# Optimization experiments

Hardware: AMD Instinct MI355X
Metric: run time of the kernel (lower is better)

Reference implementation:

```python
import jax, jax.numpy as jnp
import numpy as np

B = 8192          # batch
D = 256           # feature_dim
H = 64            # num attention heads
HD = D // H       # head_dim = 4
NC, NB, NF, NT = 2048, 2048, 512, 768
NCLS = 26
EPS = 1e-5


def _linear_params(k, out_d, in_d):
    s = 1.0 / np.sqrt(in_d)
    kw, kb = jax.random.split(k)
    W = jax.random.uniform(kw, (out_d, in_d), minval=-s, maxval=s, dtype=jnp.float32)
    b = jax.random.uniform(kb, (out_d,), minval=-s, maxval=s, dtype=jnp.float32)
    return W, b


def setup_inputs() -> dict:
    key = jax.random.key(0)
    ks = jax.random.split(key, 16)
    inp = {
        'x_context': jax.random.normal(ks[0], (B, NC), dtype=jnp.float32),
        'x_body':    jax.random.normal(ks[1], (B, NB), dtype=jnp.float32),
        'x_face':    jax.random.normal(ks[2], (B, NF), dtype=jnp.float32),
        'x_text':    jax.random.normal(ks[3], (B, NT), dtype=jnp.float32),
    }
    inp['Wc'], inp['bc'] = _linear_params(ks[4], D, NC)
    inp['Wb'], inp['bb'] = _linear_params(ks[5], D, NB)
    inp['Wf'], inp['bf'] = _linear_params(ks[6], D, NF)
    inp['Wt'], inp['bt'] = _linear_params(ks[7], D, NT)
    # MultiheadAttention packed in-proj (3D x D) and out-proj
    inp['in_w'], inp['in_b'] = _linear_params(ks[8], 3 * D, D)
    inp['out_w'], inp['out_b'] = _linear_params(ks[9], D, D)
    # gate MLP
    inp['Wg1'], inp['bg1'] = _linear_params(ks[10], D, D)
    inp['Wg2'], inp['bg2'] = _linear_params(ks[11], 1, D)
    # fusion head
    inp['W1'], inp['b1'] = _linear_params(ks[12], D, 4 * D)
    inp['gamma'] = jnp.ones((D,), dtype=jnp.float32)
    inp['beta'] = jnp.zeros((D,), dtype=jnp.float32)
    inp['W2'], inp['b2'] = _linear_params(ks[13], NCLS, D)
    return inp


def reference(x_context, x_body, x_face, x_text,
              Wc, bc, Wb, bb, Wf, bf, Wt, bt,
              in_w, in_b, out_w, out_b,
              Wg1, bg1, Wg2, bg2,
              W1, b1, gamma, beta, W2, b2):
    # per-modality projections -> [B, 4, D]
    f = jnp.stack([
        x_context @ Wc.T + bc,
        x_body    @ Wb.T + bb,
        x_face    @ Wf.T + bf,
        x_text    @ Wt.T + bt,
    ], axis=1)
    bsz = f.shape[0]

    # MultiheadAttention with seq_len=1 per token: softmax over a single key
    Wq, Wk, Wv = jnp.split(in_w, 3, axis=0)
    bq, bk, bv = jnp.split(in_b, 3)
    q = (f @ Wq.T + bq).reshape(bsz, 4, H, HD)
    k = (f @ Wk.T + bk).reshape(bsz, 4, H, HD)
    v = (f @ Wv.T + bv).reshape(bsz, 4, H, HD)
    scores = jnp.sum(q * k, axis=-1, keepdims=True) / np.sqrt(HD)  # [B,4,H,1]
    w = jax.nn.softmax(scores, axis=-1)                            # == 1 (single key)
    attn = (w * v).reshape(bsz, 4, D)
    self_out = attn @ out_w.T + out_b                              # [B,4,D]

    # cross attention: with seq_len=1 the output depends only on key/value,
    # so each (query i, key 3-j) call equals the self-style output of modality 3-j;
    # combining over the 4 key variants reduces to the mean over modalities.
    cross = jnp.mean(self_out, axis=1, keepdims=True)              # [B,1,D]

    gate = jax.nn.sigmoid(jax.nn.relu(self_out @ Wg1.T + bg1) @ Wg2.T + bg2)  # [B,4,1]
    combined = gate * self_out + (1.0 - gate) * cross              # [B,4,D]

    h = combined.reshape(bsz, 4 * D) @ W1.T + b1                   # [B,D]
    # BatchNorm1d (training-mode batch statistics, biased variance)
    mu = jnp.mean(h, axis=0)
    var = jnp.var(h, axis=0)
    h = (h - mu) / jnp.sqrt(var + EPS) * gamma + beta
    h = jax.nn.relu(h)                                             # dropout = identity (eval)
    return h @ W2.T + b2                                           # [B,26]
```

## Files before the change

### kernel.cpp

```cpp
#include <hip/hip_runtime.h>
#include <math.h>

typedef __attribute__((ext_vector_type(8))) short bf16x8;
typedef __attribute__((ext_vector_type(4))) float f32x4;
typedef unsigned short u16;
typedef unsigned int u32;

#define BSZ   8192
#define BN_EPS 1e-5f

__device__ inline u16 f2bf(float x) {
    u32 u = __float_as_uint(x);
    u32 r = (u + 0x7FFFu + ((u >> 16) & 1u)) >> 16;
    return (u16)r;
}
__device__ inline float bf2f_lo(u32 p) { return __uint_as_float(p << 16); }
__device__ inline float bf2f_hi(u32 p) { return __uint_as_float(p & 0xFFFF0000u); }

__device__ inline void async_g2l(const void* g, void* l) {
    __builtin_amdgcn_global_load_lds(
        (const __attribute__((address_space(1))) void*)g,
        (__attribute__((address_space(3))) void*)l, 16, 0, 0);
}

__global__ __launch_bounds__(256)
void wvo_kernel(const float* __restrict__ in_w, const float* __restrict__ in_b,
                const float* __restrict__ out_w, const float* __restrict__ out_b,
                float* __restrict__ wvo, float* __restrict__ bvo)
{
    const int i = blockIdx.x;
    const int j = threadIdx.x;
    const float* Wv = in_w + 512 * 256;
    float s = 0.f;
#pragma unroll 8
    for (int k = 0; k < 256; ++k)
        s = fmaf(out_w[i * 256 + k], Wv[k * 256 + j], s);
    wvo[i * 256 + j] = s;
    if (i == 0) {
        const float* bv = in_b + 512;
        float t = 0.f;
        for (int k = 0; k < 256; ++k)
            t = fmaf(out_w[j * 256 + k], bv[k], t);
        bvo[j] = t + out_b[j];
    }
}

__global__ __launch_bounds__(256)
void cvt_weights(const float* __restrict__ wvo, const float* __restrict__ Wc,
                 const float* __restrict__ Wb,  const float* __restrict__ Wf,
                 const float* __restrict__ Wt,  const float* __restrict__ Wg1,
                 const float* __restrict__ W1f, u16* __restrict__ dst)
{
    int gid = blockIdx.x * 256 + threadIdx.x;
    const float* src; u16* d; int loc;
    if      (gid <   8192) { src = wvo; d = dst + 0;       loc = gid; }
    else if (gid <  73728) { src = Wc;  d = dst + 65536;   loc = gid - 8192; }
    else if (gid < 139264) { src = Wb;  d = dst + 589824;  loc = gid - 73728; }
    else if (gid < 155648) { src = Wf;  d = dst + 1114112; loc = gid - 139264; }
    else if (gid < 180224) { src = Wt;  d = dst + 1245184; loc = gid - 155648; }
    else if (gid < 188416) { src = Wg1; d = dst + 1441792; loc = gid - 180224; }
    else                   { src = W1f; d = dst + 1507328; loc = gid - 188416; }
    const float4 v0 = *(const float4*)(src + (size_t)loc * 8);
    const float4 v1 = *(const float4*)(src + (size_t)loc * 8 + 4);
    uint4 o;
    o.x = (u32)f2bf(v0.x) | ((u32)f2bf(v0.y) << 16);
    o.y = (u32)f2bf(v0.z) | ((u32)f2bf(v0.w) << 16);
    o.z = (u32)f2bf(v1.x) | ((u32)f2bf(v1.y) << 16);
    o.w = (u32)f2bf(v1.z) | ((u32)f2bf(v1.w) << 16);
    *(uint4*)(d + (size_t)loc * 8) = o;
}

__global__ __launch_bounds__(256)
void gemm_proj(const float* __restrict__ A0, const float* __restrict__ A1,
               const float* __restrict__ A2, const float* __restrict__ A3,
               const u16* __restrict__ Wp0, const u16* __restrict__ Wp1,
               const u16* __restrict__ Wp2, const u16* __restrict__ Wp3,
               const float* __restrict__ b0, const float* __restrict__ b1,
               const float* __restrict__ b2, const float* __restrict__ b3,
               u16* __restrict__ fb)
{
    __shared__ u16 As[2][4096];
    __shared__ u16 Bs[2][16384];
    const int m = blockIdx.y;
    const float* A  = (m == 0) ? A0 : (m == 1) ? A1 : (m == 2) ? A2 : A3;
    const u16* Wp   = (m == 0) ? Wp0 : (m == 1) ? Wp1 : (m == 2) ? Wp2 : Wp3;
    const float* bi = (m == 0) ? b0 : (m == 1) ? b1 : (m == 2) ? b2 : b3;
    const int K     = (m == 0) ? 2048 : (m == 1) ? 2048 : (m == 2) ? 512 : 768;
    const int nt = K >> 6;

    const int t = threadIdx.x;
    const int w = t >> 6, l = t & 63;
    const int bm = blockIdx.x * 64;
    const int arow = t >> 2, akq = t & 3;

    float4 ar[4];
    auto loadA = [&](int k0) {
        const float* g = A + (size_t)(bm + arow) * K + k0 + akq * 16;
        ar[0] = *(const float4*)(g + 0);
        ar[1] = *(const float4*)(g + 4);
        ar[2] = *(const float4*)(g + 8);
        ar[3] = *(const float4*)(g + 12);
    };
    auto writeA = [&](int buf) {
        bf16x8 p0, p1;
        p0[0] = (short)f2bf(ar[0].x); p0[1] = (short)f2bf(ar[0].y);
        p0[2] = (short)f2bf(ar[0].z); p0[3] = (short)f2bf(ar[0].w);
        p0[4] = (short)f2bf(ar[1].x); p0[5] = (short)f2bf(ar[1].y);
        p0[6] = (short)f2bf(ar[1].z); p0[7] = (short)f2bf(ar[1].w);
        p1[0] = (short)f2bf(ar[2].x); p1[1] = (short)f2bf(ar[2].y);
        p1[2] = (short)f2bf(ar[2].z); p1[3] = (short)f2bf(ar[2].w);
        p1[4] = (short)f2bf(ar[3].x); p1[5] = (short)f2bf(ar[3].y);
        p1[6] = (short)f2bf(ar[3].z); p1[7] = (short)f2bf(ar[3].w);
        char* abw = (char*)As[buf];
        *(bf16x8*)(abw + arow * 128 + (((akq * 2 + 0) ^ (arow & 7)) << 4)) = p0;
        *(bf16x8*)(abw + arow * 128 + (((akq * 2 + 1) ^ (arow & 7)) << 4)) = p1;
    };
    auto issueB = [&](int k0, int buf) {
#pragma unroll
        for (int it = 0; it < 8; ++it) {
            const int n  = it * 32 + w * 8 + (l >> 3);
            const int ch = (l & 7) ^ (n & 7);
            async_g2l(Wp + (size_t)n * K + k0 + ch * 8, Bs[buf] + it * 2048 + w * 512);
        }
    };

    f32x4 acc[4][4];
    const f32x4 z = {0.f, 0.f, 0.f, 0.f};
#pragma unroll
    for (int i = 0; i < 4; ++i)
#pragma unroll
        for (int j = 0; j < 4; ++j) acc[i][j] = z;

    loadA(0);
    issueB(0, 0);
    writeA(0);
    __syncthreads();

    for (int t0 = 0; t0 < nt; ++t0) {
        const int cur = t0 & 1;
        if (t0 + 1 < nt) { loadA((t0 + 1) * 64); issueB((t0 + 1) * 64, cur ^ 1); }
        const char* abr = (const char*)As[cur];
        const char* bbr = (const char*)Bs[cur];
#pragma unroll
        for (int kk = 0; kk < 2; ++kk) {
            bf16x8 af[4], bq[4];
            const int ch = kk * 4 + (l >> 4);
#pragma unroll
            for (int i = 0; i < 4; ++i) {
                const int fr = i * 16 + (l & 15);
                af[i] = *(const bf16x8*)(abr + fr * 128 + ((ch ^ (fr & 7)) << 4));
            }
#pragma unroll
            for (int j = 0; j < 4; ++j) {
                const int n = w * 64 + j * 16 + (l & 15);
                bq[j] = *(const bf16x8*)(bbr + n * 128 + ((ch ^ (n & 7)) << 4));
            }
#pragma unroll
            for (int i = 0; i < 4; ++i)
#pragma unroll
                for (int j = 0; j < 4; ++j)
                    acc[i][j] = __builtin_amdgcn_mfma_f32_16x16x32_bf16(
                        af[i], bq[j], acc[i][j], 0, 0, 0);
        }
        if (t0 + 1 < nt) writeA(cur ^ 1);
        __syncthreads();
    }

#pragma unroll
    for (int j = 0; j < 4; ++j) {
        const int col = w * 64 + j * 16 + (l & 15);
        const float bv = bi[col];
#pragma unroll
        for (int i = 0; i < 4; ++i)
#pragma unroll
            for (int r = 0; r < 4; ++r) {
                const int rt = i * 16 + ((l >> 4) << 2) + r;
                fb[((size_t)(bm + rt) * 4 + m) * 256 + col] = f2bf(acc[i][j][r] + bv);
            }
    }
}

template<int EPI>
__global__ __launch_bounds__(256)
void gemm_mid(const u16* __restrict__ Ab, const u16* __restrict__ Wp,
              const float* __restrict__ bias,
              u16* __restrict__ outb, float* __restrict__ outf,
              const float* __restrict__ wg2, float* __restrict__ gpart, int K)
{
    __shared__ u16 As[2][4096];
    __shared__ u16 Bs[2][16384];
    const int t = threadIdx.x;
    const int w = t >> 6, l = t & 63;
    const int bm = blockIdx.x * 64;
    const int nt = K >> 6;

    auto issueAB = [&](int k0, int buf) {
#pragma unroll
        for (int it = 0; it < 8; ++it) {
            const int n  = it * 32 + w * 8 + (l >> 3);
            const int ch = (l & 7) ^ (n & 7);
            async_g2l(Wp + (size_t)n * K + k0 + ch * 8, Bs[buf] + it * 2048 + w * 512);
        }
#pragma unroll
        for (int it = 0; it < 2; ++it) {
            const int row = it * 32 + w * 8 + (l >> 3);
            const int ch  = (l & 7) ^ (row & 7);
            async_g2l(Ab + (size_t)(bm + row) * K + k0 + ch * 8,
                      As[buf] + it * 2048 + w * 512);
        }
    };

    f32x4 acc[4][4];
    const f32x4 z = {0.f, 0.f, 0.f, 0.f};
#pragma unroll
    for (int i = 0; i < 4; ++i)
#pragma unroll
        for (int j = 0; j < 4; ++j) acc[i][j] = z;

    issueAB(0, 0);
    __syncthreads();

    for (int t0 = 0; t0 < nt; ++t0) {
        const int cur = t0 & 1;
        if (t0 + 1 < nt) issueAB((t0 + 1) * 64, cur ^ 1);
        const char* abr = (const char*)As[cur];
        const char* bbr = (const char*)Bs[cur];
#pragma unroll
        for (int kk = 0; kk < 2; ++kk) {
            bf16x8 af[4], bq[4];
            const int ch = kk * 4 + (l >> 4);
#pragma unroll
            for (int i = 0; i < 4; ++i) {
                const int fr = i * 16 + (l & 15);
                af[i] = *(const bf16x8*)(abr + fr * 128 + ((ch ^ (fr & 7)) << 4));
            }
#pragma unroll
            for (int j = 0; j < 4; ++j) {
                const int n = w * 64 + j * 16 + (l & 15);
                bq[j] = *(const bf16x8*)(bbr + n * 128 + ((ch ^ (n & 7)) << 4));
            }
#pragma unroll
            for (int i = 0; i < 4; ++i)
#pragma unroll
                for (int j = 0; j < 4; ++j)
                    acc[i][j] = __builtin_amdgcn_mfma_f32_16x16x32_bf16(
                        af[i], bq[j], acc[i][j], 0, 0, 0);
        }
        __syncthreads();
    }

    if (EPI == 2) {
        float s[4][4];
#pragma unroll
        for (int i = 0; i < 4; ++i)
#pragma unroll
            for (int r = 0; r < 4; ++r) s[i][r] = 0.f;
#pragma unroll
        for (int j = 0; j < 4; ++j) {
            const int col = w * 64 + j * 16 + (l & 15);
            const float bv = bias[col], wv = wg2[col];
#pragma unroll
            for (int i = 0; i < 4; ++i)
#pragma unroll
                for (int r = 0; r < 4; ++r)
                    s[i][r] += fmaxf(acc[i][j][r] + bv, 0.f) * wv;
        }
#pragma unroll
        for (int off = 1; off < 16; off <<= 1)
#pragma unroll
            for (int i = 0; i < 4; ++i)
#pragma unroll
                for (int r = 0; r < 4; ++r)
                    s[i][r] += __shfl_xor(s[i][r], off);
        if ((l & 15) == 0) {
#pragma unroll
            for (int i = 0; i < 4; ++i)
#pragma unroll
                for (int r = 0; r < 4; ++r)
                    gpart[(size_t)w * 32768 + bm + i * 16 + ((l >> 4) << 2) + r] = s[i][r];
        }
    } else {
#pragma unroll
        for (int j = 0; j < 4; ++j) {
            const int col = w * 64 + j * 16 + (l & 15);
            const float bv = bias[col];
#pragma unroll
            for (int i = 0; i < 4; ++i)
#pragma unroll
                for (int r = 0; r < 4; ++r) {
                    const int rt = i * 16 + ((l >> 4) << 2) + r;
                    const float v = acc[i][j][r] + bv;
                    if (EPI == 0) outb[(size_t)(bm + rt) * 256 + col] = f2bf(v);
                    else          outf[(size_t)(bm + rt) * 256 + col] = v;
                }
        }
    }
}

__global__ __launch_bounds__(256)
void gate_fin(const float* __restrict__ gp, const float* __restrict__ bg2,
              float* __restrict__ gate)
{
    const int r = blockIdx.x * 256 + threadIdx.x;
    const float v = gp[r] + gp[32768 + r] + gp[65536 + r] + gp[98304 + r] + bg2[0];
    gate[r] = 1.f / (1.f + expf(-v));
}

__global__ __launch_bounds__(256)
void combined_k(const u16* __restrict__ so, const float* __restrict__ gate,
                u16* __restrict__ comb)
{
    const int idx = blockIdx.x * 256 + threadIdx.x;
    const int b = idx >> 7, p = idx & 127;
    const u32* s32 = (const u32*)so;
    u32* c32 = (u32*)comb;
    float lo[4], hi[4], gv[4];
#pragma unroll
    for (int m = 0; m < 4; ++m) {
        const u32 pk = s32[(size_t)(b * 4 + m) * 128 + p];
        lo[m] = bf2f_lo(pk); hi[m] = bf2f_hi(pk);
        gv[m] = gate[b * 4 + m];
    }
    const float cl = 0.25f * (lo[0] + lo[1] + lo[2] + lo[3]);
    const float ch = 0.25f * (hi[0] + hi[1] + hi[2] + hi[3]);
#pragma unroll
    for (int m = 0; m < 4; ++m) {
        const float ol = gv[m] * lo[m] + (1.f - gv[m]) * cl;
        const float oh = gv[m] * hi[m] + (1.f - gv[m]) * ch;
        c32[(size_t)b * 512 + m * 128 + p] = (u32)f2bf(ol) | ((u32)f2bf(oh) << 16);
    }
}

__global__ __launch_bounds__(256)
void bn_part(const float* __restrict__ h, float* __restrict__ psum,
             float* __restrict__ psq)
{
    const int p = blockIdx.x;
    const int d = threadIdx.x;
    float s = 0.f, q = 0.f;
#pragma unroll 8
    for (int r = 0; r < 32; ++r) {
        const float v = h[((size_t)p * 32 + r) * 256 + d];
        s += v;
        q = fmaf(v, v, q);
    }
    psum[p * 256 + d] = s;
    psq[p * 256 + d]  = q;
}

__global__ __launch_bounds__(256)
void bn_fin(const float* __restrict__ psum, const float* __restrict__ psq,
            const float* __restrict__ gamma, const float* __restrict__ beta,
            float* __restrict__ scale, float* __restrict__ shift)
{
    const int d = threadIdx.x;
    float s = 0.f, q = 0.f;
#pragma unroll 8
    for (int p = 0; p < 256; ++p) { s += psum[p * 256 + d]; q += psq[p * 256 + d]; }
    const float mu  = s * (1.f / BSZ);
    const float var = q * (1.f / BSZ) - mu * mu;
    const float inv = rsqrtf(var + BN_EPS);
    const float sc  = gamma[d] * inv;
    scale[d] = sc;
    shift[d] = beta[d] - mu * sc;
}

__global__ __launch_bounds__(256)
void final_kernel(const float* __restrict__ h, const float* __restrict__ scale,
                  const float* __restrict__ shift, const float* __restrict__ W2,
                  const float* __restrict__ b2, float* __restrict__ out)
{
    __shared__ float W2s[26][260];
    __shared__ float scs[256], shs[256];
    const int t = threadIdx.x;
    for (int u = t; u < 26 * 256; u += 256) {
        const int c = u >> 8, n = u & 255;
        W2s[c][(n >> 6) * 65 + (n & 63)] = W2[u];
    }
    scs[t] = scale[t];
    shs[t] = shift[t];
    __syncthreads();

    const int r = blockIdx.x * 64 + (t >> 2);
    const int p = t & 3;
    float acc[26];
#pragma unroll
    for (int c = 0; c < 26; ++c) acc[c] = 0.f;
    const float* hr = h + (size_t)r * 256 + p * 64;
#pragma unroll
    for (int i4 = 0; i4 < 16; ++i4) {
        const float4 v4 = *(const float4*)(hr + i4 * 4);
#pragma unroll
        for (int q = 0; q < 4; ++q) {
            const int i = i4 * 4 + q;
            const int n = p * 64 + i;
            const float vv = (q == 0) ? v4.x : (q == 1) ? v4.y : (q == 2) ? v4.z : v4.w;
            const float v = fmaxf(fmaf(vv, scs[n], shs[n]), 0.f);
            const int sw = p * 65 + i;
#pragma unroll
            for (int c = 0; c < 26; ++c)
                acc[c] = fmaf(v, W2s[c][sw], acc[c]);
        }
    }
#pragma unroll
    for (int off = 1; off < 4; off <<= 1)
#pragma unroll
        for (int c = 0; c < 26; ++c)
            acc[c] += __shfl_xor(acc[c], off);
    if (p == 0) {
#pragma unroll
        for (int c = 0; c < 26; ++c)
            out[(size_t)r * 26 + c] = acc[c] + b2[c];
    }
}

extern "C" void kernel_launch(void* const* d_in, const int* in_sizes, int n_in,
                              void* d_out, int out_size, void* d_ws, size_t ws_size,
                              hipStream_t stream)
{
    const float* x_ctx  = (const float*)d_in[0];
    const float* x_body = (const float*)d_in[1];
    const float* x_face = (const float*)d_in[2];
    const float* x_text = (const float*)d_in[3];
    const float* Wc = (const float*)d_in[4];  const float* bc = (const float*)d_in[5];
    const float* Wb = (const float*)d_in[6];  const float* bb = (const float*)d_in[7];
    const float* Wf = (const float*)d_in[8];  const float* bf = (const float*)d_in[9];
    const float* Wt = (const float*)d_in[10]; const float* bt = (const float*)d_in[11];
    const float* in_w  = (const float*)d_in[12]; const float* in_b  = (const float*)d_in[13];
    const float* out_w = (const float*)d_in[14]; const float* out_b = (const float*)d_in[15];
    const float* Wg1 = (const float*)d_in[16]; const float* bg1 = (const float*)d_in[17];
    const float* Wg2 = (const float*)d_in[18]; const float* bg2 = (const float*)d_in[19];
    const float* W1  = (const float*)d_in[20]; const float* b1  = (const float*)d_in[21];
    const float* gamma = (const float*)d_in[22]; const float* beta = (const float*)d_in[23];
    const float* W2  = (const float*)d_in[24]; const float* b2  = (const float*)d_in[25];

    char* wsb = (char*)d_ws;
    u16*   f_bf  = (u16*)(wsb + 0);
    u16*   comb  = f_bf;
    u16*   so_bf = (u16*)(wsb + (16u << 20));
    float* h     = (float*)(wsb + (16u << 20));
    u16*   wpb   = (u16*)(wsb + (32u << 20));
    float* wvo   = (float*)(wsb + (36u << 20));
    float* bvo   = (float*)(wsb + (36u << 20) + 262144);
    float* gpart = (float*)(wsb + (37u << 20));
    float* gate  = (float*)(wsb + (38u << 20));
    float* psum  = (float*)(wsb + (39u << 20));
    float* psq   = (float*)(wsb + (39u << 20) + 262144);
    float* scale = (float*)(wsb + (39u << 20) + 524288);
    float* shift = (float*)(wsb + (39u << 20) + 528384);

    u16* wvo_bf = wpb + 0;
    u16* wc_bf  = wpb + 65536;
    u16* wb_bf  = wpb + 589824;
    u16* wf_bf  = wpb + 1114112;
    u16* wt_bf  = wpb + 1245184;
    u16* wg1_bf = wpb + 1441792;
    u16* w1_bf  = wpb + 1507328;

    wvo_kernel<<<256, 256, 0, stream>>>(in_w, in_b, out_w, out_b, wvo, bvo);
    cvt_weights<<<864, 256, 0, stream>>>(wvo, Wc, Wb, Wf, Wt, Wg1, W1, wpb);

    gemm_proj<<<dim3(128, 4), 256, 0, stream>>>(x_ctx, x_body, x_face, x_text,
                                                wc_bf, wb_bf, wf_bf, wt_bf,
                                                bc, bb, bf, bt, f_bf);

    gemm_mid<0><<<512, 256, 0, stream>>>(f_bf, wvo_bf, bvo, so_bf, nullptr,
                                         nullptr, nullptr, 256);

    gemm_mid<2><<<512, 256, 0, stream>>>(so_bf, wg1_bf, bg1, nullptr, nullptr,
                                         Wg2, gpart, 256);
    gate_fin<<<128, 256, 0, stream>>>(gpart, bg2, gate);

    combined_k<<<4096, 256, 0, stream>>>(so_bf, gate, comb);

    gemm_mid<1><<<128, 256, 0, stream>>>(comb, w1_bf, b1, nullptr, h,
                                         nullptr, nullptr, 1024);

    bn_part<<<256, 256, 0, stream>>>(h, psum, psq);
    bn_fin<<<1, 256, 0, stream>>>(psum, psq, gamma, beta, scale, shift);
    final_kernel<<<128, 256, 0, stream>>>(h, scale, shift, W2, b2, (float*)d_out);
}
```

Before: 162.5 us.

## Fuse attention out-proj, gate MLP and combine into one kernel; retile GEMMs to 32 rows

The separate out-projection GEMM, gate GEMM, gate finalisation and combine kernels are merged into one fused_sgc kernel. It keeps each 32-row tile of projected features in LDS, runs both 256x256 GEMMs from it, computes the sigmoid gate in shared memory, and writes the combined tensor in place. This removes the round trips of self_out and the gate partials through global memory, plus several launches. The projection GEMM and the W1 GEMM now use 32-row tiles with a 32-wide K step and unswizzled B tiles. That doubles the grid but increases weight re-reads and may add LDS bank conflicts.

```diff
diff --git a/kernel.cpp b/kernel.cpp
--- a/kernel.cpp
+++ b/kernel.cpp
@@ -2,6 +2,7 @@
 #include <math.h>
 
 typedef __attribute__((ext_vector_type(8))) short bf16x8;
+typedef __attribute__((ext_vector_type(4))) short bf16x4;
 typedef __attribute__((ext_vector_type(4))) float f32x4;
 typedef unsigned short u16;
 typedef unsigned int u32;
@@ -79,55 +80,43 @@
                const float* __restrict__ b2, const float* __restrict__ b3,
                u16* __restrict__ fb)
 {
-    __shared__ u16 As[2][4096];
-    __shared__ u16 Bs[2][16384];
+    __shared__ u16 As[2][1024];
+    __shared__ u16 Bs[2][8192];
     const int m = blockIdx.y;
     const float* A  = (m == 0) ? A0 : (m == 1) ? A1 : (m == 2) ? A2 : A3;
     const u16* Wp   = (m == 0) ? Wp0 : (m == 1) ? Wp1 : (m == 2) ? Wp2 : Wp3;
     const float* bi = (m == 0) ? b0 : (m == 1) ? b1 : (m == 2) ? b2 : b3;
     const int K     = (m == 0) ? 2048 : (m == 1) ? 2048 : (m == 2) ? 512 : 768;
-    const int nt = K >> 6;
+    const int nt = K >> 5;
 
     const int t = threadIdx.x;
     const int w = t >> 6, l = t & 63;
-    const int bm = blockIdx.x * 64;
-    const int arow = t >> 2, akq = t & 3;
-
-    float4 ar[4];
+    const int bm = blockIdx.x * 32;
+    const int arow = t >> 3, ac4 = (t & 7) * 4;
+
+    float4 ar;
     auto loadA = [&](int k0) {
-        const float* g = A + (size_t)(bm + arow) * K + k0 + akq * 16;
-        ar[0] = *(const float4*)(g + 0);
-        ar[1] = *(const float4*)(g + 4);
-        ar[2] = *(const float4*)(g + 8);
-        ar[3] = *(const float4*)(g + 12);
+        ar = *(const float4*)(A + (size_t)(bm + arow) * K + k0 + ac4);
     };
     auto writeA = [&](int buf) {
-        bf16x8 p0, p1;
-        p0[0] = (short)f2bf(ar[0].x); p0[1] = (short)f2bf(ar[0].y);
-        p0[2] = (short)f2bf(ar[0].z); p0[3] = (short)f2bf(ar[0].w);
-        p0[4] = (short)f2bf(ar[1].x); p0[5] = (short)f2bf(ar[1].y);
-        p0[6] = (short)f2bf(ar[1].z); p0[7] = (short)f2bf(ar[1].w);
-        p1[0] = (short)f2bf(ar[2].x); p1[1] = (short)f2bf(ar[2].y);
-        p1[2] = (short)f2bf(ar[2].z); p1[3] = (short)f2bf(ar[2].w);
-        p1[4] = (short)f2bf(ar[3].x); p1[5] = (short)f2bf(ar[3].y);
-        p1[6] = (short)f2bf(ar[3].z); p1[7] = (short)f2bf(ar[3].w);
-        char* abw = (char*)As[buf];
-        *(bf16x8*)(abw + arow * 128 + (((akq * 2 + 0) ^ (arow & 7)) << 4)) = p0;
-        *(bf16x8*)(abw + arow * 128 + (((akq * 2 + 1) ^ (arow & 7)) << 4)) = p1;
+        bf16x4 p;
+        p[0] = (short)f2bf(ar.x); p[1] = (short)f2bf(ar.y);
+        p[2] = (short)f2bf(ar.z); p[3] = (short)f2bf(ar.w);
+        *(bf16x4*)((char*)As[buf] + arow * 64 + (t & 7) * 8) = p;
     };
     auto issueB = [&](int k0, int buf) {
 #pragma unroll
-        for (int it = 0; it < 8; ++it) {
-            const int n  = it * 32 + w * 8 + (l >> 3);
-            const int ch = (l & 7) ^ (n & 7);
-            async_g2l(Wp + (size_t)n * K + k0 + ch * 8, Bs[buf] + it * 2048 + w * 512);
+        for (int it = 0; it < 4; ++it) {
+            const int n0 = (w * 4 + it) * 16;
+            async_g2l(Wp + (size_t)(n0 + (l >> 2)) * K + k0 + (l & 3) * 8,
+                      Bs[buf] + n0 * 32);
         }
     };
 
-    f32x4 acc[4][4];
+    f32x4 acc[2][4];
     const f32x4 z = {0.f, 0.f, 0.f, 0.f};
 #pragma unroll
-    for (int i = 0; i < 4; ++i)
+    for (int i = 0; i < 2; ++i)
 #pragma unroll
         for (int j = 0; j < 4; ++j) acc[i][j] = z;
 
@@ -138,30 +127,22 @@
 
     for (int t0 = 0; t0 < nt; ++t0) {
         const int cur = t0 & 1;
-        if (t0 + 1 < nt) { loadA((t0 + 1) * 64); issueB((t0 + 1) * 64, cur ^ 1); }
-        const char* abr = (const char*)As[cur];
-        const char* bbr = (const char*)Bs[cur];
-#pragma unroll
-        for (int kk = 0; kk < 2; ++kk) {
-            bf16x8 af[4], bq[4];
-            const int ch = kk * 4 + (l >> 4);
-#pragma unroll
-            for (int i = 0; i < 4; ++i) {
-                const int fr = i * 16 + (l & 15);
-                af[i] = *(const bf16x8*)(abr + fr * 128 + ((ch ^ (fr & 7)) << 4));
-            }
-#pragma unroll
-            for (int j = 0; j < 4; ++j) {
-                const int n = w * 64 + j * 16 + (l & 15);
-                bq[j] = *(const bf16x8*)(bbr + n * 128 + ((ch ^ (n & 7)) << 4));
-            }
-#pragma unroll
-            for (int i = 0; i < 4; ++i)
-#pragma unroll
-                for (int j = 0; j < 4; ++j)
-                    acc[i][j] = __builtin_amdgcn_mfma_f32_16x16x32_bf16(
-                        af[i], bq[j], acc[i][j], 0, 0, 0);
-        }
+        if (t0 + 1 < nt) { loadA((t0 + 1) * 32); issueB((t0 + 1) * 32, cur ^ 1); }
+        const char* ab = (const char*)As[cur];
+        const char* bb = (const char*)Bs[cur];
+        bf16x8 af[2], bq[4];
+#pragma unroll
+        for (int i = 0; i < 2; ++i)
+            af[i] = *(const bf16x8*)(ab + (i * 16 + (l & 15)) * 64 + (l >> 4) * 16);
+#pragma unroll
+        for (int j = 0; j < 4; ++j)
+            bq[j] = *(const bf16x8*)(bb + (w * 64 + j * 16 + (l & 15)) * 64 + (l >> 4) * 16);
+#pragma unroll
+        for (int i = 0; i < 2; ++i)
+#pragma unroll
+            for (int j = 0; j < 4; ++j)
+                acc[i][j] = __builtin_amdgcn_mfma_f32_16x16x32_bf16(
+                    af[i], bq[j], acc[i][j], 0, 0, 0);
         if (t0 + 1 < nt) writeA(cur ^ 1);
         __syncthreads();
     }
@@ -171,7 +152,7 @@
         const int col = w * 64 + j * 16 + (l & 15);
         const float bv = bi[col];
 #pragma unroll
-        for (int i = 0; i < 4; ++i)
+        for (int i = 0; i < 2; ++i)
 #pragma unroll
             for (int r = 0; r < 4; ++r) {
                 const int rt = i * 16 + ((l >> 4) << 2) + r;
@@ -180,154 +161,250 @@
     }
 }
 
-template<int EPI>
-__global__ __launch_bounds__(256)
-void gemm_mid(const u16* __restrict__ Ab, const u16* __restrict__ Wp,
-              const float* __restrict__ bias,
-              u16* __restrict__ outb, float* __restrict__ outf,
-              const float* __restrict__ wg2, float* __restrict__ gpart, int K)
-{
-    __shared__ u16 As[2][4096];
-    __shared__ u16 Bs[2][16384];
-    const int t = threadIdx.x;
-    const int w = t >> 6, l = t & 63;
-    const int bm = blockIdx.x * 64;
-    const int nt = K >> 6;
-
-    auto issueAB = [&](int k0, int buf) {
-#pragma unroll
-        for (int it = 0; it < 8; ++it) {
-            const int n  = it * 32 + w * 8 + (l >> 3);
-            const int ch = (l & 7) ^ (n & 7);
-            async_g2l(Wp + (size_t)n * K + k0 + ch * 8, Bs[buf] + it * 2048 + w * 512);
-        }
-#pragma unroll
-        for (int it = 0; it < 2; ++it) {
-            const int row = it * 32 + w * 8 + (l >> 3);
-            const int ch  = (l & 7) ^ (row & 7);
-            async_g2l(Ab + (size_t)(bm + row) * K + k0 + ch * 8,
-                      As[buf] + it * 2048 + w * 512);
+__global__ __launch_bounds__(256)
+void fused_sgc(const u16* __restrict__ fb, const u16* __restrict__ wvo_bf,
+               const float* __restrict__ bvo,
+               const u16* __restrict__ wg1_bf, const float* __restrict__ bg1,
+               const float* __restrict__ wg2, const float* __restrict__ bg2,
+               u16* __restrict__ comb)
+{
+    __shared__ u16 FS[8192];
+    __shared__ u16 Bs[2][8192];
+    __shared__ float gp[4][32];
+    __shared__ float gate_s[32];
+    const int t = threadIdx.x, w = t >> 6, l = t & 63;
+    const int bm = blockIdx.x * 32;
+    char* const fs = (char*)FS;
+
+#pragma unroll
+    for (int it = 0; it < 4; ++it) {
+        const int r0 = (w * 4 + it) * 2;
+        const int row = r0 + (l >> 5);
+        const int ch = (l & 31) ^ (row & 7);
+        async_g2l(fb + (size_t)(bm + row) * 256 + ch * 8, FS + r0 * 256);
+    }
+    auto issueB = [&](const u16* Wp, int k0, int buf) {
+#pragma unroll
+        for (int it = 0; it < 4; ++it) {
+            const int n0 = (w * 4 + it) * 16;
+            async_g2l(Wp + (size_t)(n0 + (l >> 2)) * 256 + k0 + (l & 3) * 8,
+                      Bs[buf] + n0 * 32);
         }
     };
-
-    f32x4 acc[4][4];
+    issueB(wvo_bf, 0, 0);
+    __syncthreads();
+
     const f32x4 z = {0.f, 0.f, 0.f, 0.f};
-#pragma unroll
-    for (int i = 0; i < 4; ++i)
+
+    f32x4 acc[2][4];
+#pragma unroll
+    for (int i = 0; i < 2; ++i)
 #pragma unroll
         for (int j = 0; j < 4; ++j) acc[i][j] = z;
 
-    issueAB(0, 0);
-    __syncthreads();
-
-    for (int t0 = 0; t0 < nt; ++t0) {
-        const int cur = t0 & 1;
-        if (t0 + 1 < nt) issueAB((t0 + 1) * 64, cur ^ 1);
-        const char* abr = (const char*)As[cur];
-        const char* bbr = (const char*)Bs[cur];
-#pragma unroll
-        for (int kk = 0; kk < 2; ++kk) {
-            bf16x8 af[4], bq[4];
-            const int ch = kk * 4 + (l >> 4);
-#pragma unroll
-            for (int i = 0; i < 4; ++i) {
-                const int fr = i * 16 + (l & 15);
-                af[i] = *(const bf16x8*)(abr + fr * 128 + ((ch ^ (fr & 7)) << 4));
+    for (int ks = 0; ks < 8; ++ks) {
+        const int cur = ks & 1;
+        if (ks < 7) issueB(wvo_bf, (ks + 1) * 32, cur ^ 1);
+        else        issueB(wg1_bf, 0, 0);
+        bf16x8 af[2], bq[4];
+#pragma unroll
+        for (int i = 0; i < 2; ++i) {
+            const int row = i * 16 + (l & 15);
+            af[i] = *(const bf16x8*)(fs + row * 512 +
+                      (((ks * 4 + (l >> 4)) ^ (row & 7)) << 4));
+        }
+#pragma unroll
+        for (int j = 0; j < 4; ++j)
+            bq[j] = *(const bf16x8*)((char*)Bs[cur] +
+                      (w * 64 + j * 16 + (l & 15)) * 64 + (l >> 4) * 16);
+#pragma unroll
+        for (int i = 0; i < 2; ++i)
+#pragma unroll
+            for (int j = 0; j < 4; ++j)
+                acc[i][j] = __builtin_amdgcn_mfma_f32_16x16x32_bf16(
+                    af[i], bq[j], acc[i][j], 0, 0, 0);
+        __syncthreads();
+    }
+
+#pragma unroll
+    for (int j = 0; j < 4; ++j) {
+        const int col = w * 64 + j * 16 + (l & 15);
+        const float bv = bvo[col];
+#pragma unroll
+        for (int i = 0; i < 2; ++i)
+#pragma unroll
+            for (int r = 0; r < 4; ++r) {
+                const int rt = i * 16 + ((l >> 4) << 2) + r;
+                *(u16*)(fs + rt * 512 + (((col >> 3) ^ (rt & 7)) << 4) + (col & 7) * 2)
+                    = f2bf(acc[i][j][r] + bv);
             }
-#pragma unroll
-            for (int j = 0; j < 4; ++j) {
-                const int n = w * 64 + j * 16 + (l & 15);
-                bq[j] = *(const bf16x8*)(bbr + n * 128 + ((ch ^ (n & 7)) << 4));
-            }
-#pragma unroll
-            for (int i = 0; i < 4; ++i)
-#pragma unroll
-                for (int j = 0; j < 4; ++j)
-                    acc[i][j] = __builtin_amdgcn_mfma_f32_16x16x32_bf16(
-                        af[i], bq[j], acc[i][j], 0, 0, 0);
-        }
+    }
+    __syncthreads();
+
+    f32x4 g2[2][4];
+#pragma unroll
+    for (int i = 0; i < 2; ++i)
+#pragma unroll
+        for (int j = 0; j < 4; ++j) g2[i][j] = z;
+
+    for (int ks = 0; ks < 8; ++ks) {
+        const int cur = ks & 1;
+        if (ks < 7) issueB(wg1_bf, (ks + 1) * 32, cur ^ 1);
+        bf16x8 af[2], bq[4];
+#pragma unroll
+        for (int i = 0; i < 2; ++i) {
+            const int row = i * 16 + (l & 15);
+            af[i] = *(const bf16x8*)(fs + row * 512 +
+                      (((ks * 4 + (l >> 4)) ^ (row & 7)) << 4));
+        }
+#pragma unroll
+        for (int j = 0; j < 4; ++j)
+            bq[j] = *(const bf16x8*)((char*)Bs[cur] +
+                      (w * 64 + j * 16 + (l & 15)) * 64 + (l >> 4) * 16);
+#pragma unroll
+        for (int i = 0; i < 2; ++i)
+#pragma unroll
+            for (int j = 0; j < 4; ++j)
+                g2[i][j] = __builtin_amdgcn_mfma_f32_16x16x32_bf16(
+                    af[i], bq[j], g2[i][j], 0, 0, 0);
         __syncthreads();
     }
 
-    if (EPI == 2) {
-        float s[4][4];
-#pragma unroll
-        for (int i = 0; i < 4; ++i)
+    {
+        float s[2][4];
+#pragma unroll
+        for (int i = 0; i < 2; ++i)
 #pragma unroll
             for (int r = 0; r < 4; ++r) s[i][r] = 0.f;
 #pragma unroll
         for (int j = 0; j < 4; ++j) {
             const int col = w * 64 + j * 16 + (l & 15);
-            const float bv = bias[col], wv = wg2[col];
-#pragma unroll
-            for (int i = 0; i < 4; ++i)
+            const float bv = bg1[col], wv = wg2[col];
+#pragma unroll
+            for (int i = 0; i < 2; ++i)
 #pragma unroll
                 for (int r = 0; r < 4; ++r)
-                    s[i][r] += fmaxf(acc[i][j][r] + bv, 0.f) * wv;
+                    s[i][r] += fmaxf(g2[i][j][r] + bv, 0.f) * wv;
         }
 #pragma unroll
         for (int off = 1; off < 16; off <<= 1)
 #pragma unroll
-            for (int i = 0; i < 4; ++i)
+            for (int i = 0; i < 2; ++i)
 #pragma unroll
                 for (int r = 0; r < 4; ++r)
                     s[i][r] += __shfl_xor(s[i][r], off);
         if ((l & 15) == 0) {
 #pragma unroll
-            for (int i = 0; i < 4; ++i)
+            for (int i = 0; i < 2; ++i)
 #pragma unroll
                 for (int r = 0; r < 4; ++r)
-                    gpart[(size_t)w * 32768 + bm + i * 16 + ((l >> 4) << 2) + r] = s[i][r];
-        }
-    } else {
-#pragma unroll
-        for (int j = 0; j < 4; ++j) {
-            const int col = w * 64 + j * 16 + (l & 15);
-            const float bv = bias[col];
-#pragma unroll
-            for (int i = 0; i < 4; ++i)
-#pragma unroll
-                for (int r = 0; r < 4; ++r) {
-                    const int rt = i * 16 + ((l >> 4) << 2) + r;
-                    const float v = acc[i][j][r] + bv;
-                    if (EPI == 0) outb[(size_t)(bm + rt) * 256 + col] = f2bf(v);
-                    else          outf[(size_t)(bm + rt) * 256 + col] = v;
-                }
-        }
-    }
-}
-
-__global__ __launch_bounds__(256)
-void gate_fin(const float* __restrict__ gp, const float* __restrict__ bg2,
-              float* __restrict__ gate)
-{
-    const int r = blockIdx.x * 256 + threadIdx.x;
-    const float v = gp[r] + gp[32768 + r] + gp[65536 + r] + gp[98304 + r] + bg2[0];
-    gate[r] = 1.f / (1.f + expf(-v));
-}
-
-__global__ __launch_bounds__(256)
-void combined_k(const u16* __restrict__ so, const float* __restrict__ gate,
-                u16* __restrict__ comb)
-{
-    const int idx = blockIdx.x * 256 + threadIdx.x;
-    const int b = idx >> 7, p = idx & 127;
-    const u32* s32 = (const u32*)so;
-    u32* c32 = (u32*)comb;
-    float lo[4], hi[4], gv[4];
-#pragma unroll
-    for (int m = 0; m < 4; ++m) {
-        const u32 pk = s32[(size_t)(b * 4 + m) * 128 + p];
-        lo[m] = bf2f_lo(pk); hi[m] = bf2f_hi(pk);
-        gv[m] = gate[b * 4 + m];
-    }
-    const float cl = 0.25f * (lo[0] + lo[1] + lo[2] + lo[3]);
-    const float ch = 0.25f * (hi[0] + hi[1] + hi[2] + hi[3]);
-#pragma unroll
-    for (int m = 0; m < 4; ++m) {
-        const float ol = gv[m] * lo[m] + (1.f - gv[m]) * cl;
-        const float oh = gv[m] * hi[m] + (1.f - gv[m]) * ch;
-        c32[(size_t)b * 512 + m * 128 + p] = (u32)f2bf(ol) | ((u32)f2bf(oh) << 16);
+                    gp[w][i * 16 + ((l >> 4) << 2) + r] = s[i][r];
+        }
+    }
+    __syncthreads();
+    if (t < 32) {
+        const float g = gp[0][t] + gp[1][t] + gp[2][t] + gp[3][t] + bg2[0];
+        gate_s[t] = 1.f / (1.f + expf(-g));
+    }
+    __syncthreads();
+
+    u32* const comb32 = (u32*)comb;
+    const int p2 = t & 127;
+    const int gh = t >> 7;
+#pragma unroll
+    for (int gg = 0; gg < 4; ++gg) {
+        const int g = gh * 4 + gg;
+        const int d0 = p2 * 2;
+        float lo4[4], hi4[4], gv[4];
+#pragma unroll
+        for (int mm = 0; mm < 4; ++mm) {
+            const int row = g * 4 + mm;
+            const u32 v = *(const u32*)(fs + row * 512 +
+                            (((d0 >> 3) ^ (row & 7)) << 4) + (d0 & 7) * 2);
+            lo4[mm] = bf2f_lo(v); hi4[mm] = bf2f_hi(v);
+            gv[mm] = gate_s[g * 4 + mm];
+        }
+        const float cl = 0.25f * (lo4[0] + lo4[1] + lo4[2] + lo4[3]);
+        const float ch = 0.25f * (hi4[0] + hi4[1] + hi4[2] + hi4[3]);
+#pragma unroll
+        for (int mm = 0; mm < 4; ++mm) {
+            const float ol = gv[mm] * lo4[mm] + (1.f - gv[mm]) * cl;
+            const float oh = gv[mm] * hi4[mm] + (1.f - gv[mm]) * ch;
+            comb32[(size_t)(bm + g * 4 + mm) * 128 + p2] =
+                (u32)f2bf(ol) | ((u32)f2bf(oh) << 16);
+        }
+    }
+}
+
+__global__ __launch_bounds__(256)
+void gemm_w1(const u16* __restrict__ combp, const u16* __restrict__ w1p,
+             const float* __restrict__ b1p, float* __restrict__ h)
+{
+    __shared__ u16 As[2][1024];
+    __shared__ u16 Bs[2][8192];
+    const int t = threadIdx.x, w = t >> 6, l = t & 63;
+    const int bm = blockIdx.x * 32;
+    const int nt = 32;
+
+    auto issueA = [&](int k0, int buf) {
+        if (w < 2) {
+            const int r0 = w * 16;
+            async_g2l(combp + (size_t)(bm + r0 + (l >> 2)) * 1024 + k0 + (l & 3) * 8,
+                      As[buf] + r0 * 32);
+        }
+    };
+    auto issueB = [&](int k0, int buf) {
+#pragma unroll
+        for (int it = 0; it < 4; ++it) {
+            const int n0 = (w * 4 + it) * 16;
+            async_g2l(w1p + (size_t)(n0 + (l >> 2)) * 1024 + k0 + (l & 3) * 8,
+                      Bs[buf] + n0 * 32);
+        }
+    };
+
+    f32x4 acc[2][4];
+    const f32x4 z = {0.f, 0.f, 0.f, 0.f};
+#pragma unroll
+    for (int i = 0; i < 2; ++i)
+#pragma unroll
+        for (int j = 0; j < 4; ++j) acc[i][j] = z;
+
+    issueA(0, 0);
+    issueB(0, 0);
+    __syncthreads();
+
+    for (int t0 = 0; t0 < nt; ++t0) {
+        const int cur = t0 & 1;
+        if (t0 + 1 < nt) { issueA((t0 + 1) * 32, cur ^ 1); issueB((t0 + 1) * 32, cur ^ 1); }
+        const char* ab = (const char*)As[cur];
+        const char* bb = (const char*)Bs[cur];
+        bf16x8 af[2], bq[4];
+#pragma unroll
+        for (int i = 0; i < 2; ++i)
+            af[i] = *(const bf16x8*)(ab + (i * 16 + (l & 15)) * 64 + (l >> 4) * 16);
+#pragma unroll
+        for (int j = 0; j < 4; ++j)
+            bq[j] = *(const bf16x8*)(bb + (w * 64 + j * 16 + (l & 15)) * 64 + (l >> 4) * 16);
+#pragma unroll
+        for (int i = 0; i < 2; ++i)
+#pragma unroll
+            for (int j = 0; j < 4; ++j)
+                acc[i][j] = __builtin_amdgcn_mfma_f32_16x16x32_bf16(
+                    af[i], bq[j], acc[i][j], 0, 0, 0);
+        __syncthreads();
+    }
+
+#pragma unroll
+    for (int j = 0; j < 4; ++j) {
+        const int col = w * 64 + j * 16 + (l & 15);
+        const float bv = b1p[col];
+#pragma unroll
+        for (int i = 0; i < 2; ++i)
+#pragma unroll
+            for (int r = 0; r < 4; ++r) {
+                const int rt = i * 16 + ((l >> 4) << 2) + r;
+                h[(size_t)(bm + rt) * 256 + col] = acc[i][j][r] + bv;
+            }
     }
 }
 
@@ -437,17 +514,14 @@
     char* wsb = (char*)d_ws;
     u16*   f_bf  = (u16*)(wsb + 0);
     u16*   comb  = f_bf;
-    u16*   so_bf = (u16*)(wsb + (16u << 20));
     float* h     = (float*)(wsb + (16u << 20));
     u16*   wpb   = (u16*)(wsb + (32u << 20));
     float* wvo   = (float*)(wsb + (36u << 20));
     float* bvo   = (float*)(wsb + (36u << 20) + 262144);
-    float* gpart = (float*)(wsb + (37u << 20));
-    float* gate  = (float*)(wsb + (38u << 20));
-    float* psum  = (float*)(wsb + (39u << 20));
-    float* psq   = (float*)(wsb + (39u << 20) + 262144);
-    float* scale = (float*)(wsb + (39u << 20) + 524288);
-    float* shift = (float*)(wsb + (39u << 20) + 528384);
+    float* psum  = (float*)(wsb + (37u << 20));
+    float* psq   = (float*)(wsb + (37u << 20) + 262144);
+    float* scale = (float*)(wsb + (37u << 20) + 524288);
+    float* shift = (float*)(wsb + (37u << 20) + 528384);
 
     u16* wvo_bf = wpb + 0;
     u16* wc_bf  = wpb + 65536;
@@ -460,21 +534,14 @@
     wvo_kernel<<<256, 256, 0, stream>>>(in_w, in_b, out_w, out_b, wvo, bvo);
     cvt_weights<<<864, 256, 0, stream>>>(wvo, Wc, Wb, Wf, Wt, Wg1, W1, wpb);
 
-    gemm_proj<<<dim3(128, 4), 256, 0, stream>>>(x_ctx, x_body, x_face, x_text,
+    gemm_proj<<<dim3(256, 4), 256, 0, stream>>>(x_ctx, x_body, x_face, x_text,
                                                 wc_bf, wb_bf, wf_bf, wt_bf,
                                                 bc, bb, bf, bt, f_bf);
 
-    gemm_mid<0><<<512, 256, 0, stream>>>(f_bf, wvo_bf, bvo, so_bf, nullptr,
-                                         nullptr, nullptr, 256);
-
-    gemm_mid<2><<<512, 256, 0, stream>>>(so_bf, wg1_bf, bg1, nullptr, nullptr,
-                                         Wg2, gpart, 256);
-    gate_fin<<<128, 256, 0, stream>>>(gpart, bg2, gate);
-
-    combined_k<<<4096, 256, 0, stream>>>(so_bf, gate, comb);
-
-    gemm_mid<1><<<128, 256, 0, stream>>>(comb, w1_bf, b1, nullptr, h,
-                                         nullptr, nullptr, 1024);
+    fused_sgc<<<1024, 256, 0, stream>>>(f_bf, wvo_bf, bvo, wg1_bf, bg1,
+                                        Wg2, bg2, comb);
+
+    gemm_w1<<<256, 256, 0, stream>>>(comb, w1_bf, b1, h);
 
     bn_part<<<256, 256, 0, stream>>>(h, psum, psq);
     bn_fin<<<1, 256, 0, stream>>>(psum, psq, gamma, beta, scale, shift);
```

Result: slower. 170.0 us (+4.6%).
